# Kernel tuning notes

Measured on AMD Instinct MI355X. Metric: run time of the kernel, lower is better.

Reference implementation:

```python
import jax, jax.numpy as jnp
import numpy as np

N = 50000      # nodes
E = 600000     # edges
D = 128        # embedding_dimension
R = 2          # num_relations
DESC = 768; TW = 768; NUMF = 5; CATF = 3
EPS = 1e-5


def setup_inputs() -> dict:
    key = jax.random.key(0)
    ks = jax.random.split(key, 32)
    f32 = jnp.float32

    def rn(k, shape):
        return jax.random.normal(k, shape, dtype=f32)

    def w(k, fan_in, shape):
        return jax.random.normal(k, shape, dtype=f32) * (1.0 / np.sqrt(fan_in))

    inp = {}
    inp["desc_embedding"] = rn(ks[0], (N, DESC))
    inp["tweet_embedding"] = rn(ks[1], (N, TW))
    inp["num_feature"] = rn(ks[2], (N, NUMF))
    inp["cat_feature"] = rn(ks[3], (N, CATF))
    inp["edge_index"] = jax.random.randint(ks[4], (2, E), 0, N, dtype=jnp.int32)
    inp["edge_type"] = jax.random.randint(ks[5], (E,), 0, R, dtype=jnp.int32)
    q = D // 4
    inp["Wd"] = w(ks[6], DESC, (DESC, q)); inp["bd"] = jnp.zeros((q,), f32)
    inp["Wt"] = w(ks[7], TW, (TW, q));     inp["bt"] = jnp.zeros((q,), f32)
    inp["Wn"] = w(ks[8], NUMF, (NUMF, q)); inp["bn"] = jnp.zeros((q,), f32)
    inp["Wc"] = w(ks[9], CATF, (CATF, q)); inp["bc"] = jnp.zeros((q,), f32)
    inp["W1"] = w(ks[10], D, (D, D)); inp["b1"] = jnp.zeros((D,), f32)
    inp["rg1_w"] = w(ks[11], D, (R, D, D)); inp["rg1_root"] = w(ks[12], D, (D, D)); inp["rg1_bias"] = jnp.zeros((D,), f32)
    inp["ln1_g"] = jnp.ones((D,), f32); inp["ln1_b"] = jnp.zeros((D,), f32)
    inp["rg2_w"] = w(ks[13], D, (R, D, D)); inp["rg2_root"] = w(ks[14], D, (D, D)); inp["rg2_bias"] = jnp.zeros((D,), f32)
    inp["ln2_g"] = jnp.ones((D,), f32); inp["ln2_b"] = jnp.zeros((D,), f32)
    inp["W2"] = w(ks[15], D, (D, D)); inp["b2"] = jnp.zeros((D,), f32)
    inp["W3"] = w(ks[16], D, (D, 1)); inp["b3"] = jnp.zeros((1,), f32)
    return inp


def _leaky(x):
    return jnp.where(x > 0, x, 0.01 * x)


def _rgcn_max(x, edge_index, edge_type, rel_w, root_w, bias):
    # PyG RGCNConv(aggr='max'): out = x @ root + bias + sum_r (max-agg of x_j over rel-r edges) @ W_r
    src, dst = edge_index[0], edge_index[1]
    xs = x[src]  # [E, D] gathered source features
    out = x @ root_w + bias
    for r in range(R):
        msg = jnp.where((edge_type == r)[:, None], xs, -jnp.inf)
        agg = jax.ops.segment_max(msg, dst, num_segments=N)  # [N, D]
        agg = jnp.where(jnp.isinf(agg), 0.0, agg)            # empty slots -> 0
        out = out + agg @ rel_w[r]
    return out


def _graph_layernorm(x, gamma, beta):
    # torch_geometric.nn.LayerNorm, mode='graph': normalize over ALL nodes+channels of the graph
    mu = jnp.mean(x)
    xc = x - mu
    var = jnp.mean(xc * xc)
    return xc / jnp.sqrt(var + EPS) * gamma + beta


def reference(desc_embedding, tweet_embedding, num_feature, cat_feature,
              edge_index, edge_type,
              Wd, bd, Wt, bt, Wn, bn, Wc, bc,
              W1, b1, rg1_w, rg1_root, rg1_bias, ln1_g, ln1_b,
              rg2_w, rg2_root, rg2_bias, ln2_g, ln2_b,
              W2, b2, W3, b3):
    x = jnp.concatenate([
        _leaky(desc_embedding @ Wd + bd),
        _leaky(tweet_embedding @ Wt + bt),
        _leaky(num_feature @ Wn + bn),
        _leaky(cat_feature @ Wc + bc),
    ], axis=1)                                   # [N, D]
    x = _leaky(x @ W1 + b1)
    x = _rgcn_max(x, edge_index, edge_type, rg1_w, rg1_root, rg1_bias)
    x = _graph_layernorm(x, ln1_g, ln1_b)
    # dropout: eval mode (identity)
    x = _rgcn_max(x, edge_index, edge_type, rg2_w, rg2_root, rg2_bias)
    x = _graph_layernorm(x, ln2_g, ln2_b)
    x = _leaky(x @ W2 + b2)
    x = jax.nn.sigmoid(x @ W3 + b3)
    return x.reshape(-1)                          # [N]
```

## Files before the change

### kernel.cpp

```cpp
#include <hip/hip_runtime.h>
#include <cstdint>
#include <cstddef>

#define NN 50000
#define EE 600000
#define DD 128
#define NSEG (NN*2)
#define NPART ((NSEG + 255) / 256)

typedef short bf16x8 __attribute__((ext_vector_type(8)));
typedef float f32x4 __attribute__((ext_vector_type(4)));

__device__ __forceinline__ float leaky_f(float x){ return x > 0.f ? x : 0.01f*x; }

__device__ __forceinline__ unsigned short f2bf(float f){
    unsigned u = __float_as_uint(f);
    u += 0x7fffu + ((u >> 16) & 1u);
    return (unsigned short)(u >> 16);
}

__device__ __forceinline__ void split8(const float* a, bf16x8& hi, bf16x8& lo){
#pragma unroll
    for (int j=0;j<8;j++){
        unsigned u  = __float_as_uint(a[j]);
        unsigned uh = u & 0xFFFF0000u;
        hi[j] = (short)(uh >> 16);
        float lf = a[j] - __uint_as_float(uh);
        lo[j] = (short)(__float_as_uint(lf) >> 16);
    }
}


__global__ __launch_bounds__(256) void pack768_k(
    const float* __restrict__ Wd, const float* __restrict__ Wt,
    unsigned short* __restrict__ out)
{
    int idx = blockIdx.x*256 + threadIdx.x;
    int m = idx / 24576;
    int r = idx - m*24576;
    int kb   = r >> 12;
    int ks   = (r >> 10) & 3;
    int c    = (r >> 9) & 1;
    int lane = (r >> 3) & 63;
    int j    = r & 7;
    int q = lane >> 4, n16 = lane & 15;
    int k = kb*128 + ks*32 + q*8 + j;
    int n = c*16 + n16;
    const float* W = m ? Wt : Wd;
    out[idx] = f2bf(W[k*32 + n]);
}

__global__ __launch_bounds__(256) void pack128_k(
    const float* __restrict__ W0, const float* __restrict__ W1,
    const float* __restrict__ W2, const float* __restrict__ W3,
    const float* __restrict__ W4, const float* __restrict__ W5,
    const float* __restrict__ W6, const float* __restrict__ W7,
    unsigned short* __restrict__ out)
{
    int idx = blockIdx.x*256 + threadIdx.x;
    int m = idx >> 14;
    int r = idx & 16383;
    int ks   = r >> 12;
    int c    = (r >> 9) & 7;
    int lane = (r >> 3) & 63;
    int j    = r & 7;
    int q = lane >> 4, n16 = lane & 15;
    int k = ks*32 + q*8 + j;
    int n = c*16 + n16;
    const float* Ws[8] = {W0,W1,W2,W3,W4,W5,W6,W7};
    out[idx] = f2bf(Ws[m][k*128 + n]);
}

__global__ __launch_bounds__(256) void proj_k(
    const float* __restrict__ A0, const float* __restrict__ A1,
    const unsigned short* __restrict__ Bp,
    const float* __restrict__ bias0, const float* __restrict__ bias1,
    float* __restrict__ C, int M)
{
    constexpr int K = 768, CT = 2;
    const int tid = threadIdx.x;
    const int lane = tid & 63;
    const int wv = tid >> 6;
    const int q = lane >> 4, n16 = lane & 15;
    const int bm = blockIdx.x * 64;
    const int arow = bm + wv*16 + n16;
    const float* A = blockIdx.y ? A1 : A0;
    const unsigned short* bp = Bp + (size_t)blockIdx.y * 24576 + lane*8;
    const float* bias = blockIdx.y ? bias1 : bias0;
    const int c0 = blockIdx.y * 32;
    const bool rowok = arow < M;
    const float* arowp = A + (size_t)(rowok ? arow : 0) * K;

    f32x4 acc[CT];
#pragma unroll
    for (int c=0;c<CT;c++) acc[c] = (f32x4){0.f,0.f,0.f,0.f};

    float4 ar[2][8];

#define PROJ_LOADA(BUF, KB) { \
    _Pragma("unroll") \
    for (int ks=0; ks<4; ks++){ \
        const float* ap = arowp + (KB)*128 + ks*32 + q*8; \
        if (rowok){ \
            ar[BUF][ks*2]   = *reinterpret_cast<const float4*>(ap); \
            ar[BUF][ks*2+1] = *reinterpret_cast<const float4*>(ap+4); \
        } else { \
            ar[BUF][ks*2]   = make_float4(0.f,0.f,0.f,0.f); \
            ar[BUF][ks*2+1] = make_float4(0.f,0.f,0.f,0.f); \
        } \
    } }

#define PROJ_COMP(BUF, KB) { \
    bf16x8 br[8]; \
    _Pragma("unroll") \
    for (int f=0; f<8; f++) \
        br[f] = *reinterpret_cast<const bf16x8*>(bp + (size_t)((KB)*8 + f)*512); \
    _Pragma("unroll") \
    for (int ks=0; ks<4; ks++){ \
        float a[8]; \
        float4 t0 = ar[BUF][ks*2], t1 = ar[BUF][ks*2+1]; \
        a[0]=t0.x;a[1]=t0.y;a[2]=t0.z;a[3]=t0.w; \
        a[4]=t1.x;a[5]=t1.y;a[6]=t1.z;a[7]=t1.w; \
        bf16x8 ah, al; split8(a, ah, al); \
        _Pragma("unroll") \
        for (int c=0;c<CT;c++){ \
            acc[c] = __builtin_amdgcn_mfma_f32_16x16x32_bf16(ah, br[ks*2+c], acc[c], 0,0,0); \
            acc[c] = __builtin_amdgcn_mfma_f32_16x16x32_bf16(al, br[ks*2+c], acc[c], 0,0,0); \
        } \
    } }

    PROJ_LOADA(0, 0)
#pragma unroll
    for (int kb=0; kb<6; kb++){
        if (kb < 5) { PROJ_LOADA(((kb+1)&1), (kb+1)) }
        PROJ_COMP((kb&1), kb)
    }

    const int orow = bm + wv*16 + q*4;
#pragma unroll
    for (int c=0;c<CT;c++) {
        float bb = bias[c*16 + n16];
#pragma unroll
        for (int i=0;i<4;i++) {
            int r = orow + i;
            if (r < M) C[(size_t)r*DD + c0 + c*16 + n16] = leaky_f(acc[c][i] + bb);
        }
    }
#undef PROJ_LOADA
#undef PROJ_COMP
}

template<int S,int BFMASK,int LEAKY,int HEAD,int LNRED,int BI0,int BI1,int BI2>
__global__ __launch_bounds__(256) void mfgemm_k(
    const void* __restrict__ A0, const void* __restrict__ A1, const void* __restrict__ A2,
    const unsigned short* __restrict__ Bp,
    const float* __restrict__ bias, float* __restrict__ C, int M,
    const float* __restrict__ W3, const float* __restrict__ b3,
    float* __restrict__ red, float* __restrict__ outv)
{
    constexpr int CT = 8;
    const int tid = threadIdx.x;
    const int lane = tid & 63;
    const int wv = tid >> 6;
    const int q = lane >> 4, n16 = lane & 15;
    const int bm = blockIdx.x * 64;
    const int arow = bm + wv*16 + n16;
    const bool rowok = arow < M;

    f32x4 acc[CT];
#pragma unroll
    for (int c=0;c<CT;c++) acc[c] = (f32x4){0.f,0.f,0.f,0.f};

    const void* As[3] = {A0, A1, A2};
    constexpr int BI[3] = {BI0, BI1, BI2};
    const unsigned short* bpl = Bp + lane*8;

    float4 arf[2][2];
    bf16x8 arb[2];

#define MG_LOADA(BUF, SS, KS) { \
    if (!((BFMASK >> (SS)) & 1)) { \
        if (rowok){ \
            const float* ap = (const float*)As[SS] + (size_t)arow*DD + (KS)*32 + q*8; \
            arf[BUF][0] = *reinterpret_cast<const float4*>(ap); \
            arf[BUF][1] = *reinterpret_cast<const float4*>(ap+4); \
        } else { \
            arf[BUF][0] = make_float4(0.f,0.f,0.f,0.f); \
            arf[BUF][1] = make_float4(0.f,0.f,0.f,0.f); \
        } \
    } else { \
        if (rowok){ \
            const unsigned short* ap = (const unsigned short*)As[SS] + (size_t)arow*DD + (KS)*32 + q*8; \
            arb[BUF] = *reinterpret_cast<const bf16x8*>(ap); \
        } else { \
            _Pragma("unroll") for (int jj=0;jj<8;jj++) arb[BUF][jj]=0; \
        } \
    } }

#define MG_COMP(BUF, SS, KS) { \
    bf16x8 br[8]; \
    const unsigned short* bpp = bpl + BI[SS]*16384 + (KS)*4096; \
    _Pragma("unroll") \
    for (int c=0;c<8;c++) br[c] = *reinterpret_cast<const bf16x8*>(bpp + c*512); \
    if (!((BFMASK >> (SS)) & 1)) { \
        float a[8]; \
        float4 t0 = arf[BUF][0], t1 = arf[BUF][1]; \
        a[0]=t0.x;a[1]=t0.y;a[2]=t0.z;a[3]=t0.w; \
        a[4]=t1.x;a[5]=t1.y;a[6]=t1.z;a[7]=t1.w; \
        bf16x8 ah, al; split8(a, ah, al); \
        _Pragma("unroll") \
        for (int c=0;c<CT;c++){ \
            acc[c] = __builtin_amdgcn_mfma_f32_16x16x32_bf16(ah, br[c], acc[c], 0,0,0); \
            acc[c] = __builtin_amdgcn_mfma_f32_16x16x32_bf16(al, br[c], acc[c], 0,0,0); \
        } \
    } else { \
        _Pragma("unroll") \
        for (int c=0;c<CT;c++) \
            acc[c] = __builtin_amdgcn_mfma_f32_16x16x32_bf16(arb[BUF], br[c], acc[c], 0,0,0); \
    } }

    MG_LOADA(0, 0, 0)
#pragma unroll
    for (int t=0; t<S*4; t++){
        const int nt = t+1;
        if (nt < S*4) { MG_LOADA((nt&1), (nt>>2), (nt&3)) }
        MG_COMP((t&1), (t>>2), (t&3))
    }
#undef MG_LOADA
#undef MG_COMP

    const int orow = bm + wv*16 + q*4;
    if (HEAD) {
        float w3c[CT];
#pragma unroll
        for (int c=0;c<CT;c++) w3c[c] = W3[c*16 + n16];
        float bb3 = b3[0];
#pragma unroll
        for (int i=0;i<4;i++) {
            float t = 0.f;
#pragma unroll
            for (int c=0;c<CT;c++) {
                float v = acc[c][i] + bias[c*16 + n16];
                if (LEAKY) v = leaky_f(v);
                t = fmaf(v, w3c[c], t);
            }
#pragma unroll
            for (int m=1;m<16;m<<=1) t += __shfl_xor(t, m);
            int r = orow + i;
            if (n16 == 0 && r < M) outv[r] = 1.f / (1.f + expf(-(t + bb3)));
        }
    } else {
        float s = 0.f, ss = 0.f;
#pragma unroll
        for (int c=0;c<CT;c++) {
            float bb = bias[c*16 + n16];
#pragma unroll
            for (int i=0;i<4;i++) {
                int r = orow + i;
                if (r < M) {
                    float v = acc[c][i] + bb;
                    if (LEAKY) v = leaky_f(v);
                    C[(size_t)r*DD + c*16 + n16] = v;
                    if (LNRED) { s += v; ss = fmaf(v, v, ss); }
                }
            }
        }
        if (LNRED) {
#pragma unroll
            for (int o=32;o>0;o>>=1) { s += __shfl_down(s,o); ss += __shfl_down(ss,o); }
            __shared__ float rs[4], rss[4];
            if (lane == 0) { rs[wv] = s; rss[wv] = ss; }
            __syncthreads();
            if (tid == 0) {
                atomicAdd(&red[0], rs[0]+rs[1]+rs[2]+rs[3]);
                atomicAdd(&red[1], rss[0]+rss[1]+rss[2]+rss[3]);
            }
        }
    }
}

__global__ void numcat_k(const float* __restrict__ numf, const float* __restrict__ catf,
                         const float* __restrict__ Wn, const float* __restrict__ bn,
                         const float* __restrict__ Wc, const float* __restrict__ bc,
                         float* __restrict__ x)
{
    int t = blockIdx.x*blockDim.x + threadIdx.x;
    if (t >= NN*64) return;
    int n = t >> 6, c = t & 63;
    if (c < 32) {
        float acc = bn[c];
#pragma unroll
        for (int k=0;k<5;k++) acc = fmaf(numf[n*5+k], Wn[k*32+c], acc);
        x[(size_t)n*DD + 64 + c] = leaky_f(acc);
    } else {
        int cc = c - 32;
        float acc = bc[cc];
#pragma unroll
        for (int k=0;k<3;k++) acc = fmaf(catf[n*3+k], Wc[k*32+cc], acc);
        x[(size_t)n*DD + 96 + cc] = leaky_f(acc);
    }
}

__global__ void zero_int_k(int* __restrict__ p, int n)
{
    int i = blockIdx.x*blockDim.x + threadIdx.x;
    if (i < n) p[i] = 0;
}

__global__ void hist_k(const int* __restrict__ ei, const int* __restrict__ et,
                       int* __restrict__ deg)
{
    int e = blockIdx.x*blockDim.x + threadIdx.x;
    if (e >= EE) return;
    atomicAdd(&deg[ei[EE + e]*2 + et[e]], 1);
}

__global__ __launch_bounds__(256) void part_reduce_k(const int* __restrict__ deg,
                                                     int* __restrict__ part)
{
    __shared__ int s[256];
    int t = threadIdx.x;
    int i = blockIdx.x*256 + t;
    s[t] = (i < NSEG) ? deg[i] : 0;
    __syncthreads();
#pragma unroll
    for (int o=128;o>0;o>>=1) {
        if (t < o) s[t] += s[t+o];
        __syncthreads();
    }
    if (t == 0) part[blockIdx.x] = s[0];
}

__global__ __launch_bounds__(512) void part_scan_k(int* __restrict__ part)
{
    __shared__ int ps[512];
    int t = threadIdx.x;
    int v = (t < NPART) ? part[t] : 0;
    ps[t] = v; __syncthreads();
    for (int o=1;o<512;o<<=1) {
        int u = (t >= o) ? ps[t-o] : 0;
        __syncthreads();
        ps[t] += u;
        __syncthreads();
    }
    if (t < NPART) part[t] = ps[t] - v;
}

__global__ __launch_bounds__(256) void final_scan_k(const int* __restrict__ deg,
                                                    const int* __restrict__ part,
                                                    int* __restrict__ offs,
                                                    int* __restrict__ cursor)
{
    __shared__ int ps[256];
    int t = threadIdx.x;
    int i = blockIdx.x*256 + t;
    int d = (i < NSEG) ? deg[i] : 0;
    ps[t] = d; __syncthreads();
    for (int o=1;o<256;o<<=1) {
        int u = (t >= o) ? ps[t-o] : 0;
        __syncthreads();
        ps[t] += u;
        __syncthreads();
    }
    if (i < NSEG) {
        int off = part[blockIdx.x] + ps[t] - d;
        offs[i] = off; cursor[i] = off;
    }
    if (blockIdx.x == 0 && t == 0) offs[NSEG] = EE;
}

__global__ void place_k(const int* __restrict__ ei, const int* __restrict__ et,
                        int* __restrict__ cursor, unsigned short* __restrict__ csr)
{
    int e = blockIdx.x*blockDim.x + threadIdx.x;
    if (e >= EE) return;
    int r = et[e], dst = ei[EE + e], src = ei[e];
    int pos = atomicAdd(&cursor[dst*2 + r], 1);
    csr[pos] = (unsigned short)src;
}

__global__ void gather2_k(const float* __restrict__ x, const int* __restrict__ offs,
                          const unsigned short* __restrict__ csr,
                          unsigned short* __restrict__ aggb, float* __restrict__ red)
{
    if (blockIdx.x == 0 && threadIdx.x < 4) red[threadIdx.x] = 0.f;
    int seg = (blockIdx.x*blockDim.x + threadIdx.x) >> 6;
    int lane = threadIdx.x & 63;
    if (seg >= NSEG) return;
    int node = seg >> 1, r = seg & 1;
    int beg = offs[seg], end = offs[seg+1];
    float2 m = make_float2(-3.402823466e+38f, -3.402823466e+38f);
    for (int j=beg;j<end;j++) {
        int src = csr[j];
        float2 v = *reinterpret_cast<const float2*>(x + (size_t)src*DD + lane*2);
        m.x = fmaxf(m.x, v.x);
        m.y = fmaxf(m.y, v.y);
    }
    if (beg == end) { m.x = 0.f; m.y = 0.f; }
    unsigned o = (unsigned)f2bf(m.x) | ((unsigned)f2bf(m.y) << 16);
    *reinterpret_cast<unsigned*>(aggb + (size_t)r*NN*DD + (size_t)node*DD + lane*2) = o;
}

__global__ void norm_k(float* __restrict__ x, const float* __restrict__ g,
                       const float* __restrict__ b, const float* __restrict__ red)
{
    const float inv = 1.f / (float)(NN*DD);
    float mu  = red[0] * inv;
    float var = red[1] * inv - mu*mu;
    float rstd = rsqrtf(var + 1e-5f);
    int i = blockIdx.x*blockDim.x + threadIdx.x;
    int c = i & 127;
    x[i] = (x[i]-mu)*rstd*g[c] + b[c];
}

extern "C" void kernel_launch(void* const* d_in, const int* in_sizes, int n_in,
                              void* d_out, int out_size, void* d_ws, size_t ws_size,
                              hipStream_t stream)
{
    const float* desc  = (const float*)d_in[0];
    const float* tweet = (const float*)d_in[1];
    const float* numf  = (const float*)d_in[2];
    const float* catf  = (const float*)d_in[3];
    const int*   ei    = (const int*)d_in[4];
    const int*   et    = (const int*)d_in[5];
    const float* Wd=(const float*)d_in[6];  const float* bd=(const float*)d_in[7];
    const float* Wt=(const float*)d_in[8];  const float* bt=(const float*)d_in[9];
    const float* Wn=(const float*)d_in[10]; const float* bn=(const float*)d_in[11];
    const float* Wc=(const float*)d_in[12]; const float* bc=(const float*)d_in[13];
    const float* W1=(const float*)d_in[14]; const float* b1=(const float*)d_in[15];
    const float* rg1w=(const float*)d_in[16]; const float* rg1root=(const float*)d_in[17];
    const float* rg1b=(const float*)d_in[18];
    const float* ln1g=(const float*)d_in[19]; const float* ln1b=(const float*)d_in[20];
    const float* rg2w=(const float*)d_in[21]; const float* rg2root=(const float*)d_in[22];
    const float* rg2b=(const float*)d_in[23];
    const float* ln2g=(const float*)d_in[24]; const float* ln2b=(const float*)d_in[25];
    const float* W2=(const float*)d_in[26]; const float* b2=(const float*)d_in[27];
    const float* W3=(const float*)d_in[28]; const float* b3=(const float*)d_in[29];
    float* out = (float*)d_out;

    float* xa  = (float*)d_ws;
    float* xb  = xa + (size_t)NN*DD;
    unsigned short* aggb = (unsigned short*)(xb + (size_t)NN*DD);
    unsigned short* aggb0 = aggb;
    unsigned short* aggb1 = aggb + (size_t)NN*DD;
    float* red = (float*)(aggb + (size_t)2*NN*DD);
    int*   deg    = (int*)(red + 4);
    int*   offs   = deg + NSEG;
    int*   cursor = offs + NSEG + 1;
    int*   part   = cursor + NSEG;
    unsigned short* csr = (unsigned short*)(part + NPART);

    unsigned short* bp768 = (unsigned short*)deg;
    unsigned short* bp128 = bp768 + 49152;

    dim3 blk(256);
    const int mblocks = (NN + 63) / 64;
    const int nelm_blocks = (NN*DD)/256;
    const int edge_blocks = (EE+255)/256;
    const int seg_blocks  = (NSEG*64)/256;

    zero_int_k<<<(NSEG+255)/256, 256, 0, stream>>>(deg, NSEG);
    hist_k<<<edge_blocks, 256, 0, stream>>>(ei, et, deg);
    part_reduce_k<<<NPART, 256, 0, stream>>>(deg, part);
    part_scan_k<<<1, 512, 0, stream>>>(part);
    final_scan_k<<<NPART, 256, 0, stream>>>(deg, part, offs, cursor);
    place_k<<<edge_blocks, 256, 0, stream>>>(ei, et, cursor, csr);

    pack768_k<<<192, 256, 0, stream>>>(Wd, Wt, bp768);
    pack128_k<<<512, 256, 0, stream>>>(W1, rg1root, rg1w, rg1w + (size_t)DD*DD,
                                       rg2root, rg2w, rg2w + (size_t)DD*DD, W2, bp128);

    proj_k<<<dim3(mblocks,2), blk, 0, stream>>>(desc, tweet, bp768, bd, bt, xa, NN);
    numcat_k<<<(NN*64)/256, 256, 0, stream>>>(numf, catf, Wn, bn, Wc, bc, xa);

    hipLaunchKernelGGL((mfgemm_k<1,0,1,0,0,0,0,0>), dim3(mblocks), blk, 0, stream,
                       xa, nullptr, nullptr, bp128, b1, xb, NN,
                       nullptr, nullptr, nullptr, nullptr);

    gather2_k<<<seg_blocks, 256, 0, stream>>>(xb, offs, csr, aggb, red);
    hipLaunchKernelGGL((mfgemm_k<3,6,0,0,1,1,2,3>), dim3(mblocks), blk, 0, stream,
                       xb, aggb0, aggb1, bp128, rg1b, xa, NN,
                       nullptr, nullptr, red, nullptr);
    norm_k<<<nelm_blocks, 256, 0, stream>>>(xa, ln1g, ln1b, red);

    gather2_k<<<seg_blocks, 256, 0, stream>>>(xa, offs, csr, aggb, red);
    hipLaunchKernelGGL((mfgemm_k<3,6,0,0,1,4,5,6>), dim3(mblocks), blk, 0, stream,
                       xa, aggb0, aggb1, bp128, rg2b, xb, NN,
                       nullptr, nullptr, red, nullptr);
    norm_k<<<nelm_blocks, 256, 0, stream>>>(xb, ln2g, ln2b, red);

    hipLaunchKernelGGL((mfgemm_k<1,0,1,1,0,7,0,0>), dim3(mblocks), blk, 0, stream,
                       xb, nullptr, nullptr, bp128, b2, nullptr, NN,
                       W3, b3, nullptr, out);
}
```

Baseline: 765.3 us.

## Stage GEMM A-operand tiles through LDS via direct global-to-LDS loads

Replaces register-based A-tile double buffering in the projection and generic MFMA GEMM kernels with global_load_lds copies straight into shared memory. The projection kernel double-buffers 32KB LDS stages with a barrier per k-block. The generic kernel loads the whole A row block into LDS up front before computing. This aims to cut VGPR pressure and issue more loads asynchronously, at the cost of extra LDS use (up to 64-96KB per block), which may lower occupancy, plus added barriers.

```diff
diff --git a/kernel.cpp b/kernel.cpp
--- a/kernel.cpp
+++ b/kernel.cpp
@@ -10,6 +10,10 @@
 
 typedef short bf16x8 __attribute__((ext_vector_type(8)));
 typedef float f32x4 __attribute__((ext_vector_type(4)));
+
+#define GLDS16(gp, lp) __builtin_amdgcn_global_load_lds( \
+    (const __attribute__((address_space(1))) void*)(gp), \
+    (__attribute__((address_space(3))) void*)(lp), 16, 0, 0)
 
 __device__ __forceinline__ float leaky_f(float x){ return x > 0.f ? x : 0.01f*x; }
 
@@ -78,6 +82,7 @@
     float* __restrict__ C, int M)
 {
     constexpr int K = 768, CT = 2;
+    __shared__ unsigned char sm[2][32768];
     const int tid = threadIdx.x;
     const int lane = tid & 63;
     const int wv = tid >> 6;
@@ -95,30 +100,27 @@
 #pragma unroll
     for (int c=0;c<CT;c++) acc[c] = (f32x4){0.f,0.f,0.f,0.f};
 
-    float4 ar[2][8];
-
-#define PROJ_LOADA(BUF, KB) { \
+#define PSTAGE(BUF, KB) { \
     _Pragma("unroll") \
     for (int ks=0; ks<4; ks++){ \
-        const float* ap = arowp + (KB)*128 + ks*32 + q*8; \
-        if (rowok){ \
-            ar[BUF][ks*2]   = *reinterpret_cast<const float4*>(ap); \
-            ar[BUF][ks*2+1] = *reinterpret_cast<const float4*>(ap+4); \
-        } else { \
-            ar[BUF][ks*2]   = make_float4(0.f,0.f,0.f,0.f); \
-            ar[BUF][ks*2+1] = make_float4(0.f,0.f,0.f,0.f); \
+        _Pragma("unroll") \
+        for (int hf=0; hf<2; hf++){ \
+            const float* gp = arowp + (KB)*128 + ks*32 + q*8 + hf*4; \
+            GLDS16(gp, sm[BUF] + wv*8192 + ks*2048 + hf*1024); \
         } \
     } }
 
-#define PROJ_COMP(BUF, KB) { \
+#define PCOMP(BUF, KB) { \
     bf16x8 br[8]; \
     _Pragma("unroll") \
     for (int f=0; f<8; f++) \
         br[f] = *reinterpret_cast<const bf16x8*>(bp + (size_t)((KB)*8 + f)*512); \
     _Pragma("unroll") \
     for (int ks=0; ks<4; ks++){ \
+        const unsigned char* ab = sm[BUF] + wv*8192 + ks*2048 + lane*16; \
+        float4 t0 = *reinterpret_cast<const float4*>(ab); \
+        float4 t1 = *reinterpret_cast<const float4*>(ab + 1024); \
         float a[8]; \
-        float4 t0 = ar[BUF][ks*2], t1 = ar[BUF][ks*2+1]; \
         a[0]=t0.x;a[1]=t0.y;a[2]=t0.z;a[3]=t0.w; \
         a[4]=t1.x;a[5]=t1.y;a[6]=t1.z;a[7]=t1.w; \
         bf16x8 ah, al; split8(a, ah, al); \
@@ -129,11 +131,12 @@
         } \
     } }
 
-    PROJ_LOADA(0, 0)
+    PSTAGE(0, 0)
 #pragma unroll
     for (int kb=0; kb<6; kb++){
-        if (kb < 5) { PROJ_LOADA(((kb+1)&1), (kb+1)) }
-        PROJ_COMP((kb&1), kb)
+        __syncthreads();
+        if (kb < 5) { PSTAGE(((kb+1)&1), (kb+1)) }
+        PCOMP((kb&1), kb)
     }
 
     const int orow = bm + wv*16 + q*4;
@@ -146,8 +149,8 @@
             if (r < M) C[(size_t)r*DD + c0 + c*16 + n16] = leaky_f(acc[c][i] + bb);
         }
     }
-#undef PROJ_LOADA
-#undef PROJ_COMP
+#undef PSTAGE
+#undef PCOMP
 }
 
 template<int S,int BFMASK,int LEAKY,int HEAD,int LNRED,int BI0,int BI1,int BI2>
@@ -159,6 +162,12 @@
     float* __restrict__ red, float* __restrict__ outv)
 {
     constexpr int CT = 8;
+    constexpr int sz0 = ((BFMASK>>0)&1) ? 16384 : 32768;
+    constexpr int sz1 = (S>1) ? ((((BFMASK)>>1)&1) ? 16384 : 32768) : 0;
+    constexpr int sz2 = (S>2) ? ((((BFMASK)>>2)&1) ? 16384 : 32768) : 0;
+    __shared__ unsigned char sm[sz0+sz1+sz2];
+    const int sbase[3] = {0, sz0, sz0+sz1};
+
     const int tid = threadIdx.x;
     const int lane = tid & 63;
     const int wv = tid >> 6;
@@ -166,6 +175,7 @@
     const int bm = blockIdx.x * 64;
     const int arow = bm + wv*16 + n16;
     const bool rowok = arow < M;
+    const int arowc = rowok ? arow : 0;
 
     f32x4 acc[CT];
 #pragma unroll
@@ -175,59 +185,54 @@
     constexpr int BI[3] = {BI0, BI1, BI2};
     const unsigned short* bpl = Bp + lane*8;
 
-    float4 arf[2][2];
-    bf16x8 arb[2];
-
-#define MG_LOADA(BUF, SS, KS) { \
-    if (!((BFMASK >> (SS)) & 1)) { \
-        if (rowok){ \
-            const float* ap = (const float*)As[SS] + (size_t)arow*DD + (KS)*32 + q*8; \
-            arf[BUF][0] = *reinterpret_cast<const float4*>(ap); \
-            arf[BUF][1] = *reinterpret_cast<const float4*>(ap+4); \
-        } else { \
-            arf[BUF][0] = make_float4(0.f,0.f,0.f,0.f); \
-            arf[BUF][1] = make_float4(0.f,0.f,0.f,0.f); \
-        } \
-    } else { \
-        if (rowok){ \
-            const unsigned short* ap = (const unsigned short*)As[SS] + (size_t)arow*DD + (KS)*32 + q*8; \
-            arb[BUF] = *reinterpret_cast<const bf16x8*>(ap); \
-        } else { \
-            _Pragma("unroll") for (int jj=0;jj<8;jj++) arb[BUF][jj]=0; \
-        } \
-    } }
-
-#define MG_COMP(BUF, SS, KS) { \
-    bf16x8 br[8]; \
-    const unsigned short* bpp = bpl + BI[SS]*16384 + (KS)*4096; \
-    _Pragma("unroll") \
-    for (int c=0;c<8;c++) br[c] = *reinterpret_cast<const bf16x8*>(bpp + c*512); \
-    if (!((BFMASK >> (SS)) & 1)) { \
-        float a[8]; \
-        float4 t0 = arf[BUF][0], t1 = arf[BUF][1]; \
-        a[0]=t0.x;a[1]=t0.y;a[2]=t0.z;a[3]=t0.w; \
-        a[4]=t1.x;a[5]=t1.y;a[6]=t1.z;a[7]=t1.w; \
-        bf16x8 ah, al; split8(a, ah, al); \
-        _Pragma("unroll") \
-        for (int c=0;c<CT;c++){ \
-            acc[c] = __builtin_amdgcn_mfma_f32_16x16x32_bf16(ah, br[c], acc[c], 0,0,0); \
-            acc[c] = __builtin_amdgcn_mfma_f32_16x16x32_bf16(al, br[c], acc[c], 0,0,0); \
-        } \
-    } else { \
-        _Pragma("unroll") \
-        for (int c=0;c<CT;c++) \
-            acc[c] = __builtin_amdgcn_mfma_f32_16x16x32_bf16(arb[BUF], br[c], acc[c], 0,0,0); \
-    } }
-
-    MG_LOADA(0, 0, 0)
+#pragma unroll
+    for (int s=0; s<S; s++){
+        if (!((BFMASK >> s) & 1)) {
+#pragma unroll
+            for (int ks=0; ks<4; ks++){
+#pragma unroll
+                for (int hf=0; hf<2; hf++){
+                    const float* gp = (const float*)As[s] + (size_t)arowc*DD + ks*32 + q*8 + hf*4;
+                    GLDS16(gp, sm + sbase[s] + wv*8192 + ks*2048 + hf*1024);
+                }
+            }
+        } else {
+#pragma unroll
+            for (int ks=0; ks<4; ks++){
+                const unsigned short* gp = (const unsigned short*)As[s] + (size_t)arowc*DD + ks*32 + q*8;
+                GLDS16(gp, sm + sbase[s] + wv*4096 + ks*1024);
+            }
+        }
+    }
+    __syncthreads();
+
 #pragma unroll
     for (int t=0; t<S*4; t++){
-        const int nt = t+1;
-        if (nt < S*4) { MG_LOADA((nt&1), (nt>>2), (nt&3)) }
-        MG_COMP((t&1), (t>>2), (t&3))
-    }
-#undef MG_LOADA
-#undef MG_COMP
+        const int SS = t>>2, KS = t&3;
+        bf16x8 br[8];
+        const unsigned short* bpp = bpl + BI[SS]*16384 + KS*4096;
+#pragma unroll
+        for (int c=0;c<8;c++) br[c] = *reinterpret_cast<const bf16x8*>(bpp + c*512);
+        if (!((BFMASK >> SS) & 1)) {
+            const unsigned char* ab = sm + sbase[SS] + wv*8192 + KS*2048 + lane*16;
+            float4 t0 = *reinterpret_cast<const float4*>(ab);
+            float4 t1 = *reinterpret_cast<const float4*>(ab + 1024);
+            float a[8];
+            a[0]=t0.x;a[1]=t0.y;a[2]=t0.z;a[3]=t0.w;
+            a[4]=t1.x;a[5]=t1.y;a[6]=t1.z;a[7]=t1.w;
+            bf16x8 ah, al; split8(a, ah, al);
+#pragma unroll
+            for (int c=0;c<CT;c++){
+                acc[c] = __builtin_amdgcn_mfma_f32_16x16x32_bf16(ah, br[c], acc[c], 0,0,0);
+                acc[c] = __builtin_amdgcn_mfma_f32_16x16x32_bf16(al, br[c], acc[c], 0,0,0);
+            }
+        } else {
+            bf16x8 arb = *reinterpret_cast<const bf16x8*>(sm + sbase[SS] + wv*4096 + KS*1024 + lane*16);
+#pragma unroll
+            for (int c=0;c<CT;c++)
+                acc[c] = __builtin_amdgcn_mfma_f32_16x16x32_bf16(arb, br[c], acc[c], 0,0,0);
+        }
+    }
 
     const int orow = bm + wv*16 + q*4;
     if (HEAD) {
```

New measurement: 785.3 us. +2.6%, slower.
